# Optimization experiments

Measured on AMD Instinct MI355X. Metric: run time of the kernel, lower is better.

Reference implementation:

```python
import jax, jax.numpy as jnp
import numpy as np

# module constants (from init_kwargs)
R_EQ = 1.0
WELL_DEPTH = 1.0
CUTOFF = 2.5
HEAL = 0.5

N_EDGES = 20_000_000
N_ATOMS = 1_000_000
N_MOL = 1000


def setup_inputs() -> dict:
    key = jax.random.key(0)
    k1, k2 = jax.random.split(key)
    vec_ij = jax.random.normal(k1, (N_EDGES, 3), dtype=jnp.float32)
    positions = jax.random.normal(k2, (N_ATOMS, 3), dtype=jnp.float32)
    idx_i = jax.random.randint(jax.random.fold_in(key, 1), (N_EDGES,), 0, N_ATOMS, dtype=jnp.int32)
    # sorted molecule indices covering [0, N_MOL), last element == N_MOL-1
    idx_m = (jnp.arange(N_ATOMS, dtype=jnp.int32) * N_MOL // N_ATOMS).astype(jnp.int32)
    return {"vec_ij": vec_ij, "positions": positions, "idx_i": idx_i, "idx_m": idx_m}


def reference(vec_ij, positions, idx_i, idx_m):
    # per-edge distance [E,1]
    r = jnp.linalg.norm(vec_ij, axis=1, keepdims=True)
    # CustomCutoff switching function
    t = (r - (CUTOFF - HEAL)) / HEAL
    r_function = 1.0 + t * t * (2.0 * t - 3.0)
    switch = jnp.where(r > CUTOFF - HEAL, r_function, jnp.ones_like(r))
    switch = jnp.where(r > CUTOFF, jnp.zeros_like(r), switch)
    # LJ pair energy
    power_6 = (R_EQ / r) ** 6
    power_12 = power_6 * power_6
    yij = (power_12 - power_6) * switch  # [E,1]
    # scatter-add edges -> atoms
    yi = jax.ops.segment_sum(yij, idx_i, num_segments=positions.shape[0])  # [N,1]
    # index-add atoms -> molecules
    y = jax.ops.segment_sum(yi, idx_m, num_segments=N_MOL)  # [M,1]
    y = jnp.squeeze(y, -1)
    return WELL_DEPTH * 0.5 * y
```

## Files before the change

kernel.cpp:

```cpp
#include <hip/hip_runtime.h>

#define RCUT   2.5f
#define RIN    2.0f
#define INVH   2.0f

#define BT     512
#define NF4    (BT * 3)

__device__ __forceinline__ float lj_edge(float x, float y, float z) {
    float r2 = fmaf(x, x, fmaf(y, y, z * z));
    float r  = sqrtf(r2);
    if (r > RCUT) return 0.0f;
    float inv2 = 1.0f / r2;
    float p6   = inv2 * inv2 * inv2;
    float sw   = 1.0f;
    if (r > RIN) {
        float t = (r - RIN) * INVH;
        sw = fmaf(t * t, fmaf(2.0f, t, -3.0f), 1.0f);
    }
    return (p6 * p6 - p6) * sw;
}

__device__ __forceinline__ int mol_of(int a, int n_mol,
                                      unsigned long long M, int sh,
                                      bool uni, const int* __restrict__ bounds) {
    unsigned q = (unsigned)a * (unsigned)n_mol;
    int g = (int)(((unsigned long long)q * M) >> sh);
    if (!uni) {
        if (g > n_mol - 1) g = n_mol - 1;
        if (g < 0) g = 0;
        while (g > 0 && a < bounds[g]) --g;
        while (g < n_mol - 1 && a >= bounds[g + 1]) ++g;
    }
    return g;
}

__global__ __launch_bounds__(256) void init_k(float* __restrict__ out, int n_mol,
                                              int* __restrict__ flag, int flag_init) {
    int i = blockIdx.x * 256 + threadIdx.x;
    if (i < n_mol) out[i] = 0.0f;
    if (i == 0) *flag = flag_init;
}

__global__ __launch_bounds__(256) void build_bounds(
    const int* __restrict__ idx_m, int* __restrict__ start,
    int* __restrict__ flag, int n_atoms, int n_mol) {
    int a = blockIdx.x * 256 + threadIdx.x;
    if (a >= n_atoms) return;
    int m  = idx_m[a];
    int pm = (a == 0) ? -1 : idx_m[a - 1];
    for (int mm = pm + 1; mm <= m; ++mm) start[mm] = a;
    if (a == n_atoms - 1)
        for (int mm = m + 1; mm <= n_mol; ++mm) start[mm] = n_atoms;
    int mf = (int)(((unsigned long long)(unsigned)a * (unsigned)n_mol) / (unsigned)n_atoms);
    if (m != mf) atomicAnd(flag, 0);
}

__global__ __launch_bounds__(BT) void lj_main(
    const float4* __restrict__ vec4,
    const int4*   __restrict__ idx4,
    const int*    __restrict__ bounds_g,
    const int*    __restrict__ flag,
    const float*  __restrict__ vec,
    const int*    __restrict__ idx_i,
    float*        __restrict__ out,
    int n_edges, int n_mol,
    unsigned long long M, int sh)
{
    extern __shared__ char smem[];
    float4* stage  = (float4*)smem;
    float*  bins   = (float*)(smem + NF4 * 16);
    int*    bounds = (int*)(smem + NF4 * 16 + n_mol * 4);

    for (int i = threadIdx.x; i < n_mol; i += BT) bins[i] = 0.0f;
    for (int i = threadIdx.x; i <= n_mol; i += BT) bounds[i] = bounds_g[i];
    const bool uni = (*flag != 0);
    __syncthreads();

    const int n_g     = n_edges >> 2;
    const int nf4_tot = n_g * 3;
    const int nchunks = (n_g + BT - 1) / BT;
    const int t = threadIdx.x;

    for (int ch = blockIdx.x; ch < nchunks; ch += gridDim.x) {
        const int gbase = ch * BT;
        const int fb    = gbase * 3;
        #pragma unroll
        for (int j = 0; j < 3; ++j) {
            int fi = fb + j * BT + t;
            if (fi < nf4_tot) stage[j * BT + t] = vec4[fi];
        }
        __syncthreads();

        const int g = gbase + t;
        if (g < n_g) {
            float4 A = stage[3 * t + 0];
            float4 B = stage[3 * t + 1];
            float4 C = stage[3 * t + 2];
            int4  ii = idx4[g];

            float y0 = lj_edge(A.x, A.y, A.z);
            float y1 = lj_edge(A.w, B.x, B.y);
            float y2 = lj_edge(B.z, B.w, C.x);
            float y3 = lj_edge(C.y, C.z, C.w);

            if (y0 != 0.0f) atomicAdd(&bins[mol_of(ii.x, n_mol, M, sh, uni, bounds)], y0);
            if (y1 != 0.0f) atomicAdd(&bins[mol_of(ii.y, n_mol, M, sh, uni, bounds)], y1);
            if (y2 != 0.0f) atomicAdd(&bins[mol_of(ii.z, n_mol, M, sh, uni, bounds)], y2);
            if (y3 != 0.0f) atomicAdd(&bins[mol_of(ii.w, n_mol, M, sh, uni, bounds)], y3);
        }
        __syncthreads();
    }

    if (blockIdx.x == 0 && t < (n_edges & 3)) {
        int e = 4 * n_g + t;
        float v = lj_edge(vec[3 * e], vec[3 * e + 1], vec[3 * e + 2]);
        if (v != 0.0f) atomicAdd(&bins[mol_of(idx_i[e], n_mol, M, sh, uni, bounds)], v);
    }
    __syncthreads();

    int off = (int)((blockIdx.x * 131u) % (unsigned)n_mol);
    for (int i = threadIdx.x; i < n_mol; i += BT) {
        int j = i + off; if (j >= n_mol) j -= n_mol;
        float v = bins[j];
        if (v != 0.0f) atomicAdd(&out[j], 0.5f * v);
    }
}

extern "C" void kernel_launch(void* const* d_in, const int* in_sizes, int n_in,
                              void* d_out, int out_size, void* d_ws, size_t ws_size,
                              hipStream_t stream) {
    const float* vec   = (const float*)d_in[0];
    const int*   idx_i = (const int*)d_in[2];
    const int*   idx_m = (const int*)d_in[3];
    float*       out   = (float*)d_out;

    const int n_edges = in_sizes[2];
    const int n_atoms = in_sizes[3];
    const int n_mol   = out_size;

    int* start = (int*)d_ws;
    int* flag  = (int*)d_ws + (n_mol + 2);

    unsigned d = (unsigned)n_atoms;
    unsigned long long M = 1; int sh = 32;
    bool ok = ((unsigned long long)(unsigned)n_mol * d) <= 0x7fffffffull;
    if (ok) {
        bool found = false;
        for (sh = 32; sh <= 62; ++sh) {
            unsigned long long tk = 1ull << sh;
            M = tk / d + 1;
            unsigned long long e = M * d - tk;
            if (e <= (1ull << (sh - 31))) { found = true; break; }
        }
        ok = found;
    }
    if (!ok) { M = 0; sh = 0; }

    init_k<<<(n_mol + 255) / 256, 256, 0, stream>>>(out, n_mol, flag, ok ? 1 : 0);
    build_bounds<<<(n_atoms + 255) / 256, 256, 0, stream>>>(idx_m, start, flag, n_atoms, n_mol);

    const int    nb  = 1024;
    const size_t lds = (size_t)NF4 * 16 + (size_t)n_mol * 4 + (size_t)(n_mol + 1) * 4;
    lj_main<<<nb, BT, lds, stream>>>(
        (const float4*)vec, (const int4*)idx_i, start, flag,
        vec, idx_i, out, n_edges, n_mol, M, sh);
}
```

Measured before the change: 408.6 us.

## Replace LDS-staged float4 loads with direct per-edge loads and fast math

Drops the shared-memory staging of vec as float4 and the per-chunk barriers. Each thread now reads one edge as a 12-byte struct and one index directly from global memory in a grid-stride loop. It also uses squared-distance cutoff tests, hardware rcp/sqrt intrinsics and a branchless switch, and reads molecule bounds from global memory instead of LDS. This trades wider vectorized loads for simpler control flow and fewer syncs, at the risk of less efficient 12-byte accesses and slightly lower precision from the approximate rcp.

```diff
diff --git a/kernel.cpp b/kernel.cpp
--- a/kernel.cpp
+++ b/kernel.cpp
@@ -1,39 +1,10 @@
 #include <hip/hip_runtime.h>
 
-#define RCUT   2.5f
-#define RIN    2.0f
-#define INVH   2.0f
+#define RCUT2  6.25f
+#define RIN2   4.0f
+#define BT     512
 
-#define BT     512
-#define NF4    (BT * 3)
-
-__device__ __forceinline__ float lj_edge(float x, float y, float z) {
-    float r2 = fmaf(x, x, fmaf(y, y, z * z));
-    float r  = sqrtf(r2);
-    if (r > RCUT) return 0.0f;
-    float inv2 = 1.0f / r2;
-    float p6   = inv2 * inv2 * inv2;
-    float sw   = 1.0f;
-    if (r > RIN) {
-        float t = (r - RIN) * INVH;
-        sw = fmaf(t * t, fmaf(2.0f, t, -3.0f), 1.0f);
-    }
-    return (p6 * p6 - p6) * sw;
-}
-
-__device__ __forceinline__ int mol_of(int a, int n_mol,
-                                      unsigned long long M, int sh,
-                                      bool uni, const int* __restrict__ bounds) {
-    unsigned q = (unsigned)a * (unsigned)n_mol;
-    int g = (int)(((unsigned long long)q * M) >> sh);
-    if (!uni) {
-        if (g > n_mol - 1) g = n_mol - 1;
-        if (g < 0) g = 0;
-        while (g > 0 && a < bounds[g]) --g;
-        while (g < n_mol - 1 && a >= bounds[g + 1]) ++g;
-    }
-    return g;
-}
+struct __attribute__((aligned(4))) F3 { float x, y, z; };
 
 __global__ __launch_bounds__(256) void init_k(float* __restrict__ out, int n_mol,
                                               int* __restrict__ flag, int flag_init) {
@@ -56,74 +27,54 @@
     if (m != mf) atomicAnd(flag, 0);
 }
 
-__global__ __launch_bounds__(BT) void lj_main(
-    const float4* __restrict__ vec4,
-    const int4*   __restrict__ idx4,
-    const int*    __restrict__ bounds_g,
-    const int*    __restrict__ flag,
-    const float*  __restrict__ vec,
-    const int*    __restrict__ idx_i,
-    float*        __restrict__ out,
+__global__ __launch_bounds__(BT) void lj_direct(
+    const F3*  __restrict__ vec3,
+    const int* __restrict__ idx_i,
+    const int* __restrict__ bounds_g,
+    const int* __restrict__ flag,
+    float*     __restrict__ out,
     int n_edges, int n_mol,
     unsigned long long M, int sh)
 {
-    extern __shared__ char smem[];
-    float4* stage  = (float4*)smem;
-    float*  bins   = (float*)(smem + NF4 * 16);
-    int*    bounds = (int*)(smem + NF4 * 16 + n_mol * 4);
-
+    extern __shared__ float bins[];
     for (int i = threadIdx.x; i < n_mol; i += BT) bins[i] = 0.0f;
-    for (int i = threadIdx.x; i <= n_mol; i += BT) bounds[i] = bounds_g[i];
     const bool uni = (*flag != 0);
     __syncthreads();
 
-    const int n_g     = n_edges >> 2;
-    const int nf4_tot = n_g * 3;
-    const int nchunks = (n_g + BT - 1) / BT;
-    const int t = threadIdx.x;
+    const int stride = gridDim.x * BT;
+    for (int e = blockIdx.x * BT + threadIdx.x; e < n_edges; e += stride) {
+        F3  v = vec3[e];
+        int a = idx_i[e];
 
-    for (int ch = blockIdx.x; ch < nchunks; ch += gridDim.x) {
-        const int gbase = ch * BT;
-        const int fb    = gbase * 3;
-        #pragma unroll
-        for (int j = 0; j < 3; ++j) {
-            int fi = fb + j * BT + t;
-            if (fi < nf4_tot) stage[j * BT + t] = vec4[fi];
+        float r2 = fmaf(v.x, v.x, fmaf(v.y, v.y, v.z * v.z));
+        if (r2 > RCUT2) continue;
+
+        float inv2 = __builtin_amdgcn_rcpf(r2);
+        float p6   = inv2 * inv2 * inv2;
+        float y    = fmaf(p6, p6, -p6);
+
+        float r  = __builtin_amdgcn_sqrtf(r2);
+        float t  = fmaf(2.0f, r, -4.0f);
+        float sw = fmaf(t * t, fmaf(2.0f, t, -3.0f), 1.0f);
+        y *= (r2 > RIN2) ? sw : 1.0f;
+
+        unsigned q = (unsigned)a * (unsigned)n_mol;
+        int m = (int)(((unsigned long long)q * M) >> sh);
+        if (!uni) {
+            if (m > n_mol - 1) m = n_mol - 1;
+            if (m < 0) m = 0;
+            while (m > 0 && a < bounds_g[m]) --m;
+            while (m < n_mol - 1 && a >= bounds_g[m + 1]) ++m;
         }
-        __syncthreads();
-
-        const int g = gbase + t;
-        if (g < n_g) {
-            float4 A = stage[3 * t + 0];
-            float4 B = stage[3 * t + 1];
-            float4 C = stage[3 * t + 2];
-            int4  ii = idx4[g];
-
-            float y0 = lj_edge(A.x, A.y, A.z);
-            float y1 = lj_edge(A.w, B.x, B.y);
-            float y2 = lj_edge(B.z, B.w, C.x);
-            float y3 = lj_edge(C.y, C.z, C.w);
-
-            if (y0 != 0.0f) atomicAdd(&bins[mol_of(ii.x, n_mol, M, sh, uni, bounds)], y0);
-            if (y1 != 0.0f) atomicAdd(&bins[mol_of(ii.y, n_mol, M, sh, uni, bounds)], y1);
-            if (y2 != 0.0f) atomicAdd(&bins[mol_of(ii.z, n_mol, M, sh, uni, bounds)], y2);
-            if (y3 != 0.0f) atomicAdd(&bins[mol_of(ii.w, n_mol, M, sh, uni, bounds)], y3);
-        }
-        __syncthreads();
+        atomicAdd(&bins[m], y);
     }
 
-    if (blockIdx.x == 0 && t < (n_edges & 3)) {
-        int e = 4 * n_g + t;
-        float v = lj_edge(vec[3 * e], vec[3 * e + 1], vec[3 * e + 2]);
-        if (v != 0.0f) atomicAdd(&bins[mol_of(idx_i[e], n_mol, M, sh, uni, bounds)], v);
-    }
     __syncthreads();
-
-    int off = (int)((blockIdx.x * 131u) % (unsigned)n_mol);
+    unsigned off = (blockIdx.x * 131u) % (unsigned)n_mol;
     for (int i = threadIdx.x; i < n_mol; i += BT) {
-        int j = i + off; if (j >= n_mol) j -= n_mol;
-        float v = bins[j];
-        if (v != 0.0f) atomicAdd(&out[j], 0.5f * v);
+        int j = i + (int)off; if (j >= n_mol) j -= n_mol;
+        float bv = bins[j];
+        if (bv != 0.0f) atomicAdd(&out[j], 0.5f * bv);
     }
 }
 
@@ -161,8 +112,7 @@
     build_bounds<<<(n_atoms + 255) / 256, 256, 0, stream>>>(idx_m, start, flag, n_atoms, n_mol);
 
     const int    nb  = 1024;
-    const size_t lds = (size_t)NF4 * 16 + (size_t)n_mol * 4 + (size_t)(n_mol + 1) * 4;
-    lj_main<<<nb, BT, lds, stream>>>(
-        (const float4*)vec, (const int4*)idx_i, start, flag,
-        vec, idx_i, out, n_edges, n_mol, M, sh);
+    const size_t lds = (size_t)n_mol * sizeof(float);
+    lj_direct<<<nb, BT, lds, stream>>>(
+        (const F3*)vec, idx_i, start, flag, out, n_edges, n_mol, M, sh);
 }
```

Result: faster. 399.4 us (-2.3%).
